# Kernel optimization log

Measured on AMD Instinct MI355X. Metric: run time of the kernel, lower is better.

The kernel has to match this reference:

```python
import jax, jax.numpy as jnp
import numpy as np

DIM = 512; HEADS = 8; HD = DIM // HEADS
B = 4; H = 32; W = 32; TXT = 77; LAT = 512
NE = 8; HID = 4 * DIM

def _ln(x, g, b):
    mu = jnp.mean(x, -1, keepdims=True)
    v = jnp.mean((x - mu) ** 2, -1, keepdims=True)
    return (x - mu) * jax.lax.rsqrt(v + 1e-5) * g + b

def _mha(q, k, v, in_w, in_b, out_w, out_b):
    # torch nn.MultiheadAttention (batch_first): packed in_proj, scaled dot-product, out_proj
    wq, wk, wv = jnp.split(in_w, 3, axis=0)
    bq, bk, bv = jnp.split(in_b, 3)
    sp = lambda t: t.reshape(t.shape[0], t.shape[1], HEADS, HD)
    Q = sp(q @ wq.T + bq) * (HD ** -0.5)
    K = sp(k @ wk.T + bk)
    V = sp(v @ wv.T + bv)
    att = jax.nn.softmax(jnp.einsum('bqhd,bkhd->bhqk', Q, K), axis=-1)
    o = jnp.einsum('bhqk,bkhd->bqhd', att, V).reshape(q.shape[0], q.shape[1], DIM)
    return o @ out_w.T + out_b

def _modconv1x1(x, weight, mod_w, mod_b, w_lat):
    # ModulatedConv with kernel_size=1: per-sample modulated + demodulated 1x1 conv == batched matmul
    style = w_lat @ mod_w.T + mod_b              # [B, Cin]
    wt = weight[None] * style[:, None, :]        # [B, Cout, Cin]
    wt = wt * jax.lax.rsqrt(jnp.sum(wt ** 2, axis=2, keepdims=True) + 1e-8)
    return jnp.einsum('boi,bihw->bohw', wt, x)

def _forward(x, w, text_seq, pin_weight, pin_mod_w, pin_mod_b, pout_weight, pout_mod_w, pout_mod_b,
             ln1_g, ln1_b, ln2_g, ln2_b, ln3_g, ln3_b,
             sa_in_w, sa_in_b, sa_out_w, sa_out_b, ca_in_w, ca_in_b, ca_out_w, ca_out_b,
             r_feat_mu, r_text_mu, r_comb_mu, r_temp, e_w1, e_b1, e_w2, e_b2):
    x_in = _modconv1x1(x, pin_weight, pin_mod_w, pin_mod_b, w)
    x_flat = x_in.transpose(0, 2, 3, 1).reshape(B, H * W, DIM)
    xn = _ln(x_flat, ln1_g, ln1_b)
    x_flat = x_flat + _mha(xn, xn, xn, sa_in_w, sa_in_b, sa_out_w, sa_out_b)
    xn = _ln(x_flat, ln2_g, ln2_b)
    x_flat = x_flat + _mha(xn, text_seq, text_seq, ca_in_w, ca_in_b, ca_out_w, ca_out_b)
    # SparseMoE (eval mode): Bayesian router uses mean weights, hard top-1 one-hot routing
    tok = _ln(x_flat, ln3_g, ln3_b).reshape(B * H * W, DIM)
    w_tok = jnp.repeat(w, H * W, axis=0)                      # [N, LAT]
    combined = jnp.concatenate([tok @ r_feat_mu, w_tok @ r_text_mu], axis=1)  # [N, 256]
    logits = (combined @ r_comb_mu) / jnp.clip(r_temp, 0.1, None)
    probs = jax.nn.softmax(logits, axis=1)
    one_hot = jax.nn.one_hot(jnp.argmax(probs, axis=1), NE, dtype=probs.dtype)  # [N, NE]
    hdn = jax.nn.gelu(jnp.einsum('nd,edh->neh', tok, e_w1) + e_b1, approximate=False)
    expert_out = jnp.einsum('neh,ehd->ned', hdn, e_w2) + e_b2  # [N, NE, DIM]
    moe = jnp.einsum('ne,ned->nd', one_hot, expert_out)
    x_flat = x_flat + moe.reshape(B, H * W, DIM)
    x_sp = x_flat.reshape(B, H, W, DIM).transpose(0, 3, 1, 2)
    x_out = _modconv1x1(x_sp, pout_weight, pout_mod_w, pout_mod_b, w)
    return x_out, one_hot

def setup_inputs():
    key = jax.random.key(0)
    ks = jax.random.split(key, 20)
    r = lambda i, shape, s=1.0: jax.random.normal(ks[i], shape, jnp.float32) * s
    z = lambda *shape: jnp.zeros(shape, jnp.float32)
    o = lambda *shape: jnp.ones(shape, jnp.float32)
    return {
        'x': r(0, (B, DIM, H, W)),
        'w': r(1, (B, LAT)),
        'text_seq': r(2, (B, TXT, DIM)),
        'pin_weight': r(3, (DIM, DIM), 0.05), 'pin_mod_w': r(4, (DIM, LAT), 0.02), 'pin_mod_b': z(DIM),
        'pout_weight': r(5, (DIM, DIM), 0.05), 'pout_mod_w': r(6, (DIM, LAT), 0.02), 'pout_mod_b': z(DIM),
        'ln1_g': o(DIM), 'ln1_b': z(DIM), 'ln2_g': o(DIM), 'ln2_b': z(DIM), 'ln3_g': o(DIM), 'ln3_b': z(DIM),
        'sa_in_w': r(7, (3 * DIM, DIM), 0.03), 'sa_in_b': z(3 * DIM),
        'sa_out_w': r(8, (DIM, DIM), 0.03), 'sa_out_b': z(DIM),
        'ca_in_w': r(9, (3 * DIM, DIM), 0.03), 'ca_in_b': z(3 * DIM),
        'ca_out_w': r(10, (DIM, DIM), 0.03), 'ca_out_b': z(DIM),
        'r_feat_mu': r(11, (DIM, 128), 0.1), 'r_text_mu': r(12, (LAT, 128), 0.1),
        'r_comb_mu': r(13, (256, NE), 0.1), 'r_temp': o(1),
        'e_w1': r(14, (NE, DIM, HID), 0.02), 'e_b1': z(NE, HID),
        'e_w2': r(15, (NE, HID, DIM), 0.02), 'e_b2': z(NE, DIM),
    }

def reference(x, w, text_seq, pin_weight, pin_mod_w, pin_mod_b, pout_weight, pout_mod_w, pout_mod_b,
              ln1_g, ln1_b, ln2_g, ln2_b, ln3_g, ln3_b,
              sa_in_w, sa_in_b, sa_out_w, sa_out_b, ca_in_w, ca_in_b, ca_out_w, ca_out_b,
              r_feat_mu, r_text_mu, r_comb_mu, r_temp, e_w1, e_b1, e_w2, e_b2):
    return _forward(x, w, text_seq, pin_weight, pin_mod_w, pin_mod_b, pout_weight, pout_mod_w, pout_mod_b,
                    ln1_g, ln1_b, ln2_g, ln2_b, ln3_g, ln3_b,
                    sa_in_w, sa_in_b, sa_out_w, sa_out_b, ca_in_w, ca_in_b, ca_out_w, ca_out_b,
                    r_feat_mu, r_text_mu, r_comb_mu, r_temp, e_w1, e_b1, e_w2, e_b2)
```

## Files before the change

kernel.cpp:

```cpp
#include <hip/hip_runtime.h>
#include <hip/hip_bf16.h>
#include <math.h>

#define DIMC 512
#define HEADS 8
#define HD 64
#define BB 4
#define HWX 1024
#define TXT 77
#define LATC 512
#define NE 8
#define HIDC 2048
#define NTOK 4096
#define MAXT 72

typedef __attribute__((ext_vector_type(8))) short bf16x8;
typedef __attribute__((ext_vector_type(4))) float f32x4;
typedef __hip_bfloat16 bf16;

__device__ __forceinline__ void split2(float v, bf16& h, bf16& l) {
    h = __float2bfloat16(v);
    l = __float2bfloat16(v - __bfloat162float(h));
}
__device__ __forceinline__ void split2s(float v, short& h, short& l) {
// ... 180 lines not shown
        *(bf16x8*)&BsL[bufo + t * 8] = vbl;
        __syncthreads();
        int kn = (kk + 32 < K) ? kk + 32 : kk;
        bf16x8 nah = *(const bf16x8*)(AbH + aoff + kn);
        bf16x8 nal = *(const bf16x8*)(AbL + aoff + kn);
        bf16x8 nbh = *(const bf16x8*)(BbH + boff + kn);
        bf16x8 nbl = *(const bf16x8*)(BbL + boff + kn);
        bf16x8 aH[2], aL[2], bH[2], bL[2];
        #pragma unroll
        for (int i = 0; i < 2; i++) {
            aH[i] = *(const bf16x8*)&AsH[bufo + aOff[i]];
            aL[i] = *(const bf16x8*)&AsL[bufo + aOff[i]];
            bH[i] = *(const bf16x8*)&BsH[bufo + bOff[i]];
            bL[i] = *(const bf16x8*)&BsL[bufo + bOff[i]];
        }
        #pragma unroll
        for (int i = 0; i < 2; i++)
        #pragma unroll
        for (int j = 0; j < 2; j++) {
            acc[i][j] = __builtin_amdgcn_mfma_f32_16x16x32_bf16(aH[i], bH[j], acc[i][j], 0, 0, 0);
            acc[i][j] = __builtin_amdgcn_mfma_f32_16x16x32_bf16(aH[i], bL[j], acc[i][j], 0, 0, 0);
            acc[i][j] = __builtin_amdgcn_mfma_f32_16x16x32_bf16(aL[i], bH[j], acc[i][j], 0, 0, 0);
        }
        vah = nah; val = nal; vbh = nbh; vbl = nbl;
        bufo ^= 2048;
    }
    #pragma unroll
    for (int i = 0; i < 2; i++)
    #pragma unroll
    for (int j = 0; j < 2; j++)
    #pragma unroll
    for (int r = 0; r < 4; r++) {
        int row = bm + wm + i * 16 + fq * 4 + r;
        int col = bn + wn + j * 16 + fr;
        if (row < M) {
            long off = (long)row * cs_m + (long)col * cs_n;
            float v = acc[i][j][r];
            if (bias) v += bias[col];
            if (Oh) {
                bf16 hh, ll; split2(v, hh, ll);
                Oh[off] = hh; Ol[off] = ll;
            } else {
                if (Rb) v += Rb[off];
                Cb[off] = v;
            }
        }
    }
}

__global__ __launch_bounds__(256) void mgemm128x64_kernel(
    const bf16* __restrict__ Ah, const bf16* __restrict__ Al,
    const bf16* __restrict__ Bh, const bf16* __restrict__ Bl,
    const float* __restrict__ bias, bf16* __restrict__ Oh, bf16* __restrict__ Ol,
    int M, int N, int K) {
    __shared__ short AsH[2 * 4096];
    __shared__ short AsL[2 * 4096];
    __shared__ short BsH[2 * 2048];
    __shared__ short BsL[2 * 2048];
    const short* AbH = (const short*)Ah;
    const short* AbL = (const short*)Al;
    const short* BbH = (const short*)Bh;
    const short* BbL = (const short*)Bl;
    int bm = blockIdx.y * 128, bn = blockIdx.x * 64;
    int t = threadIdx.x, lane = t & 63, w = t >> 6;
    int wm = (w >> 1) * 64, wn = (w & 1) * 32;
    int p0 = t, p1 = t + 256;
    int ra0 = p0 >> 2, ka0 = (p0 & 3) ^ ((ra0 >> 1) & 3);
    int ra1 = p1 >> 2, ka1 = (p1 & 3) ^ ((ra1 >> 1) & 3);
    int arow0 = bm + ra0; if (arow0 > M - 1) arow0 = M - 1;
    int arow1 = bm + ra1; if (arow1 > M - 1) arow1 = M - 1;
    long aoff0 = (long)arow0 * K + ka0 * 8;
    long aoff1 = (long)arow1 * K + ka1 * 8;
    int rb = t >> 2, kb2 = (t & 3) ^ ((rb >> 1) & 3);
    long boff = (long)(bn + rb) * K + kb2 * 8;
    int fr = lane & 15, fq = lane >> 4;
    int aOff[4], bOff[2];
    #pragma unroll
    for (int i = 0; i < 4; i++) {
        int row = wm + i * 16 + fr;
        aOff[i] = row * 32 + ((fq ^ ((row >> 1) & 3)) * 8);
    }
    #pragma unroll
    for (int j = 0; j < 2; j++) {
        int col = wn + j * 16 + fr;
        bOff[j] = col * 32 + ((fq ^ ((col >> 1) & 3)) * 8);
    }
    f32x4 acc[4][2] = {};
    bf16x8 vah0 = *(const bf16x8*)(AbH + aoff0);
    bf16x8 vah1 = *(const bf16x8*)(AbH + aoff1);
    bf16x8 val0 = *(const bf16x8*)(AbL + aoff0);
    bf16x8 val1 = *(const bf16x8*)(AbL + aoff1);
    bf16x8 vbh  = *(const bf16x8*)(BbH + boff);
    bf16x8 vbl  = *(const bf16x8*)(BbL + boff);
    int bufA = 0, bufB = 0;
    for (int kk = 0; kk < K; kk += 32) {
        *(bf16x8*)&AsH[bufA + p0 * 8] = vah0;  *(bf16x8*)&AsH[bufA + p1 * 8] = vah1;
        *(bf16x8*)&AsL[bufA + p0 * 8] = val0;  *(bf16x8*)&AsL[bufA + p1 * 8] = val1;
        *(bf16x8*)&BsH[bufB + t * 8] = vbh;
        *(bf16x8*)&BsL[bufB + t * 8] = vbl;
        __syncthreads();
        int kn = (kk + 32 < K) ? kk + 32 : kk;
        bf16x8 nah0 = *(const bf16x8*)(AbH + aoff0 + kn);
        bf16x8 nah1 = *(const bf16x8*)(AbH + aoff1 + kn);
        bf16x8 nal0 = *(const bf16x8*)(AbL + aoff0 + kn);
        bf16x8 nal1 = *(const bf16x8*)(AbL + aoff1 + kn);
        bf16x8 nbh  = *(const bf16x8*)(BbH + boff + kn);
        bf16x8 nbl  = *(const bf16x8*)(BbL + boff + kn);
        bf16x8 aH[4], aL[4], bH[2], bL[2];
        #pragma unroll
        for (int i = 0; i < 4; i++) {
            aH[i] = *(const bf16x8*)&AsH[bufA + aOff[i]];
            aL[i] = *(const bf16x8*)&AsL[bufA + aOff[i]];
        }
        #pragma unroll
        for (int j = 0; j < 2; j++) {
            bH[j] = *(const bf16x8*)&BsH[bufB + bOff[j]];
            bL[j] = *(const bf16x8*)&BsL[bufB + bOff[j]];
        }
        #pragma unroll
        for (int i = 0; i < 4; i++)
        #pragma unroll
        for (int j = 0; j < 2; j++) {
            acc[i][j] = __builtin_amdgcn_mfma_f32_16x16x32_bf16(aH[i], bH[j], acc[i][j], 0, 0, 0);
            acc[i][j] = __builtin_amdgcn_mfma_f32_16x16x32_bf16(aH[i], bL[j], acc[i][j], 0, 0, 0);
            acc[i][j] = __builtin_amdgcn_mfma_f32_16x16x32_bf16(aL[i], bH[j], acc[i][j], 0, 0, 0);
        }
        vah0 = nah0; vah1 = nah1; val0 = nal0; val1 = nal1;
        vbh = nbh; vbl = nbl;
        bufA ^= 4096; bufB ^= 2048;
    }
    #pragma unroll
    for (int i = 0; i < 4; i++)
    #pragma unroll
    for (int j = 0; j < 2; j++)
    #pragma unroll
    for (int r = 0; r < 4; r++) {
        int row = bm + wm + i * 16 + fq * 4 + r;
        int col = bn + wn + j * 16 + fr;
        if (row < M) {
            long off = (long)row * N + col;
            float v = acc[i][j][r] + bias[col];
            bf16 hh, ll; split2(v, hh, ll);
            Oh[off] = hh; Ol[off] = ll;
        }
    }
}

__global__ __launch_bounds__(256) void sa_mfma_kernel(
    const bf16* __restrict__ qh, const bf16* __restrict__ ql,
    bf16* __restrict__ oh, bf16* __restrict__ ol) {
    int qt = blockIdx.x, h = blockIdx.y, b = blockIdx.z;
    __shared__ short KsH[4096], KsL[4096];
    __shared__ short VtH[4608], VtL[4608];
    __shared__ short PHs[4][1024], PLs[4][1024];
    int t = threadIdx.x, lane = t & 63, w = t >> 6;
    int fr = lane & 15, fq = lane >> 4;
    const short* QH = (const short*)qh;
    const short* QL = (const short*)ql;
    long qrow = (long)(b * 1024 + qt * 64 + w * 16 + fr) * 1536 + h * 64;
    bf16x8 Qh2[2], Ql2[2];
    Qh2[0] = *(const bf16x8*)(QH + qrow + fq * 8);
    Qh2[1] = *(const bf16x8*)(QH + qrow + 32 + fq * 8);
    Ql2[0] = *(const bf16x8*)(QL + qrow + fq * 8);
    Ql2[1] = *(const bf16x8*)(QL + qrow + 32 + fq * 8);
    float l_i[4] = {0.f, 0.f, 0.f, 0.f};
    f32x4 o_acc[4] = {};
    int c0 = t, c1 = t + 256;
    int r0 = c0 >> 3, g0 = c0 & 7;
    int r1 = c1 >> 3, g1 = c1 & 7;
    int kd0 = r0 * 64 + ((g0 * 8) ^ ((r0 & 7) << 3));
    int kd1 = r1 * 64 + ((g1 * 8) ^ ((r1 & 7) << 3));
    long kb = (long)(b * 1024) * 1536 + 512 + h * 64;
    long vb = kb + 512;
    long lo0 = (long)r0 * 1536 + g0 * 8, lo1 = (long)r1 * 1536 + g1 * 8;
    short* ph = PHs[w]; short* pl = PLs[w];
    bf16x8 kh0 = *(const bf16x8*)(QH + kb + lo0);
    bf16x8 kh1 = *(const bf16x8*)(QH + kb + lo1);
    bf16x8 kl0 = *(const bf16x8*)(QL + kb + lo0);
    bf16x8 kl1 = *(const bf16x8*)(QL + kb + lo1);
    bf16x8 vh0 = *(const bf16x8*)(QH + vb + lo0);
    bf16x8 vh1 = *(const bf16x8*)(QH + vb + lo1);
    bf16x8 vl0 = *(const bf16x8*)(QL + vb + lo0);
    bf16x8 vl1 = *(const bf16x8*)(QL + vb + lo1);
    for (int kt = 0; kt < 16; kt++) {
        __syncthreads();
        *(bf16x8*)&KsH[kd0] = kh0;  *(bf16x8*)&KsH[kd1] = kh1;
        *(bf16x8*)&KsL[kd0] = kl0;  *(bf16x8*)&KsL[kd1] = kl1;
        #pragma unroll
        for (int j = 0; j < 8; j++) {
            int d0 = g0 * 8 + j;
            int i0 = d0 * 72 + (r0 ^ (g0 << 3));
            VtH[i0] = ((short*)&vh0)[j];  VtL[i0] = ((short*)&vl0)[j];
            int d1 = g1 * 8 + j;
            int i1 = d1 * 72 + (r1 ^ (g1 << 3));
            VtH[i1] = ((short*)&vh1)[j];  VtL[i1] = ((short*)&vl1)[j];
        }
        __syncthreads();
        int ktn = (kt + 1 < 16) ? kt + 1 : kt;
        long ko = kb + (long)(ktn * 64) * 1536;
        long vo = vb + (long)(ktn * 64) * 1536;
        bf16x8 nkh0 = *(const bf16x8*)(QH + ko + lo0);
        bf16x8 nkh1 = *(const bf16x8*)(QH + ko + lo1);
        bf16x8 nkl0 = *(const bf16x8*)(QL + ko + lo0);
        bf16x8 nkl1 = *(const bf16x8*)(QL + ko + lo1);
        bf16x8 nvh0 = *(const bf16x8*)(QH + vo + lo0);
        bf16x8 nvh1 = *(const bf16x8*)(QH + vo + lo1);
        bf16x8 nvl0 = *(const bf16x8*)(QL + vo + lo0);
        bf16x8 nvl1 = *(const bf16x8*)(QL + vo + lo1);
        __builtin_amdgcn_s_setprio(1);
        f32x4 s[4] = {};
        #pragma unroll
        for (int cf = 0; cf < 4; cf++) {
            int kvrow = cf * 16 + fr;
            #pragma unroll
            for (int kf = 0; kf < 2; kf++) {
                int idx = kvrow * 64 + ((kf * 32 + fq * 8) ^ ((kvrow & 7) << 3));
                bf16x8 Bh2 = *(const bf16x8*)&KsH[idx];
                bf16x8 Bl2 = *(const bf16x8*)&KsL[idx];
                s[cf] = __builtin_amdgcn_mfma_f32_16x16x32_bf16(Qh2[kf], Bh2, s[cf], 0, 0, 0);
                s[cf] = __builtin_amdgcn_mfma_f32_16x16x32_bf16(Qh2[kf], Bl2, s[cf], 0, 0, 0);
                s[cf] = __builtin_amdgcn_mfma_f32_16x16x32_bf16(Ql2[kf], Bh2, s[cf], 0, 0, 0);
            }
        }
        __builtin_amdgcn_s_setprio(0);
        #pragma unroll
        for (int cf = 0; cf < 4; cf++)
        #pragma unroll
        for (int reg = 0; reg < 4; reg++) {
            float e = __expf(s[cf][reg] * 0.125f);
            s[cf][reg] = e;
            l_i[reg] += e;
        }
        #pragma unroll
        for (int cf = 0; cf < 4; cf++)
        #pragma unroll
        for (int reg = 0; reg < 4; reg++) {
            int q = fq * 4 + reg, kv = cf * 16 + fr;
            int idx = q * 64 + (kv ^ ((q & 7) << 3));
            split2s(s[cf][reg], ph[idx], pl[idx]);
        }
        asm volatile("s_waitcnt lgkmcnt(0)" ::: "memory");
        __builtin_amdgcn_sched_barrier(0);
        __builtin_amdgcn_s_setprio(1);
        bf16x8 Pf_h[2], Pf_l[2];
        #pragma unroll
        for (int kf = 0; kf < 2; kf++) {
            int idx = fr * 64 + ((kf * 32 + fq * 8) ^ ((fr & 7) << 3));
            Pf_h[kf] = *(const bf16x8*)&ph[idx];
            Pf_l[kf] = *(const bf16x8*)&pl[idx];
        }
        #pragma unroll
        for (int cf = 0; cf < 4; cf++) {
            int d = cf * 16 + fr;
            #pragma unroll
            for (int kf = 0; kf < 2; kf++) {
                int idx = d * 72 + ((kf * 32 + fq * 8) ^ (((d >> 3) & 7) << 3));
                bf16x8 Vh2 = *(const bf16x8*)&VtH[idx];
                bf16x8 Vl2 = *(const bf16x8*)&VtL[idx];
                o_acc[cf] = __builtin_amdgcn_mfma_f32_16x16x32_bf16(Pf_h[kf], Vh2, o_acc[cf], 0, 0, 0);
                o_acc[cf] = __builtin_amdgcn_mfma_f32_16x16x32_bf16(Pf_h[kf], Vl2, o_acc[cf], 0, 0, 0);
                o_acc[cf] = __builtin_amdgcn_mfma_f32_16x16x32_bf16(Pf_l[kf], Vh2, o_acc[cf], 0, 0, 0);
            }
        }
        __builtin_amdgcn_s_setprio(0);
        kh0 = nkh0; kh1 = nkh1; kl0 = nkl0; kl1 = nkl1;
        vh0 = nvh0; vh1 = nvh1; vl0 = nvl0; vl1 = nvl1;
    }
    #pragma unroll
    for (int reg = 0; reg < 4; reg++) {
        float rs = l_i[reg];
        rs += __shfl_xor(rs, 1);
        rs += __shfl_xor(rs, 2);
        rs += __shfl_xor(rs, 4);
        rs += __shfl_xor(rs, 8);
        float inv = 1.f / rs;
        long m = (long)(b * 1024 + qt * 64 + w * 16 + fq * 4 + reg);
        #pragma unroll
        for (int cf = 0; cf < 4; cf++) {
            float v = o_acc[cf][reg] * inv;
            bf16 hh, ll; split2(v, hh, ll);
            long off = m * DIMC + h * 64 + cf * 16 + fr;
            oh[off] = hh; ol[off] = ll;
        }
    }
}

__global__ __launch_bounds__(256) void ca_mfma_kernel(
    const bf16* __restrict__ qh, const bf16* __restrict__ ql,
    const bf16* __restrict__ kvh, const bf16* __restrict__ kvl,
    bf16* __restrict__ oh, bf16* __restrict__ ol) {
    int qt = blockIdx.x, h = blockIdx.y, b = blockIdx.z;
    __shared__ short UH[8192], UL[8192];
    __shared__ short PHs[4][2048], PLs[4][2048];
    int t = threadIdx.x, lane = t & 63, w = t >> 6;
    int fr = lane & 15, fq = lane >> 4;
    const short* QH = (const short*)qh;
    const short* QL = (const short*)ql;
    const short* KVH = (const short*)kvh;
    const short* KVL = (const short*)kvl;
    long qrow = (long)(b * 1024 + qt * 64 + w * 16 + fr) * DIMC + h * 64;
    bf16x8 Qh2[2], Ql2[2];
    Qh2[0] = *(const bf16x8*)(QH + qrow + fq * 8);
    Qh2[1] = *(const bf16x8*)(QH + qrow + 32 + fq * 8);
    Ql2[0] = *(const bf16x8*)(QL + qrow + fq * 8);
    Ql2[1] = *(const bf16x8*)(QL + qrow + 32 + fq * 8);
    for (int c = t; c < 768; c += 256) {
        int r = c >> 3, g = c & 7;
        int idx = r * 64 + ((g * 8) ^ ((r & 7) << 3));
        bf16x8 vh = {}, vl = {};
        if (r < 77) {
            long src = (long)(b * 77 + r) * 1024 + h * 64 + g * 8;
            vh = *(const bf16x8*)(KVH + src);
            vl = *(const bf16x8*)(KVL + src);
        }
        *(bf16x8*)&UH[idx] = vh;
        *(bf16x8*)&UL[idx] = vl;
    }
    __syncthreads();
    f32x4 s[5] = {};
    #pragma unroll
    for (int cf = 0; cf < 5; cf++) {
        int kvrow = cf * 16 + fr;
        #pragma unroll
        for (int kf = 0; kf < 2; kf++) {
            int idx = kvrow * 64 + ((kf * 32 + fq * 8) ^ ((kvrow & 7) << 3));
            bf16x8 Bh2 = *(const bf16x8*)&UH[idx];
            bf16x8 Bl2 = *(const bf16x8*)&UL[idx];
            s[cf] = __builtin_amdgcn_mfma_f32_16x16x32_bf16(Qh2[kf], Bh2, s[cf], 0, 0, 0);
            s[cf] = __builtin_amdgcn_mfma_f32_16x16x32_bf16(Qh2[kf], Bl2, s[cf], 0, 0, 0);
            s[cf] = __builtin_amdgcn_mfma_f32_16x16x32_bf16(Ql2[kf], Bh2, s[cf], 0, 0, 0);
        }
    }
    float inv[4];
    #pragma unroll
    for (int reg = 0; reg < 4; reg++) {
        float rs = 0.f;
        #pragma unroll
        for (int cf = 0; cf < 5; cf++) {
            int kv = cf * 16 + fr;
            float e = (kv < 77) ? __expf(s[cf][reg] * 0.125f) : 0.f;
            s[cf][reg] = e;
            rs += e;
        }
        rs += __shfl_xor(rs, 1);
        rs += __shfl_xor(rs, 2);
        rs += __shfl_xor(rs, 4);
        rs += __shfl_xor(rs, 8);
        inv[reg] = 1.f / rs;
    }
    short* ph = PHs[w]; short* pl = PLs[w];
    #pragma unroll
    for (int cf = 0; cf < 6; cf++)
    #pragma unroll
    for (int reg = 0; reg < 4; reg++) {
        int q = fq * 4 + reg, kv = cf * 16 + fr;
        int idx = q * 128 + (kv ^ ((q & 7) << 3));
        float pv = (cf < 5) ? s[cf][reg] * inv[reg] : 0.f;
        split2s(pv, ph[idx], pl[idx]);
    }
    __syncthreads();
    for (int c = t; c < 768; c += 256) {
        int r = c >> 3, g = c & 7;
        bf16x8 vh = {}, vl = {};
        if (r < 77) {
            long src = (long)(b * 77 + r) * 1024 + 512 + h * 64 + g * 8;
            vh = *(const bf16x8*)(KVH + src);
            vl = *(const bf16x8*)(KVL + src);
        }
        #pragma unroll
        for (int j = 0; j < 8; j++) {
            int d = g * 8 + j;
            int idx = d * 128 + (r ^ (((d >> 3) & 7) << 3));
            UH[idx] = ((short*)&vh)[j];
            UL[idx] = ((short*)&vl)[j];
        }
    }
    __syncthreads();
    f32x4 o_acc[4] = {};
    bf16x8 Pf_h[3], Pf_l[3];
    #pragma unroll
    for (int kf = 0; kf < 3; kf++) {
        int idx = fr * 128 + ((kf * 32 + fq * 8) ^ ((fr & 7) << 3));
        Pf_h[kf] = *(const bf16x8*)&ph[idx];
        Pf_l[kf] = *(const bf16x8*)&pl[idx];
    }
    #pragma unroll
    for (int cf = 0; cf < 4; cf++) {
        int d = cf * 16 + fr;
        #pragma unroll
        for (int kf = 0; kf < 3; kf++) {
            int idx = d * 128 + ((kf * 32 + fq * 8) ^ (((d >> 3) & 7) << 3));
            bf16x8 Vh2 = *(const bf16x8*)&UH[idx];
            bf16x8 Vl2 = *(const bf16x8*)&UL[idx];
            o_acc[cf] = __builtin_amdgcn_mfma_f32_16x16x32_bf16(Pf_h[kf], Vh2, o_acc[cf], 0, 0, 0);
            o_acc[cf] = __builtin_amdgcn_mfma_f32_16x16x32_bf16(Pf_h[kf], Vl2, o_acc[cf], 0, 0, 0);
            o_acc[cf] = __builtin_amdgcn_mfma_f32_16x16x32_bf16(Pf_l[kf], Vh2, o_acc[cf], 0, 0, 0);
        }
    }
    #pragma unroll
    for (int reg = 0; reg < 4; reg++) {
        long m = (long)(b * 1024 + qt * 64 + w * 16 + fq * 4 + reg);
        #pragma unroll
        for (int cf = 0; cf < 4; cf++) {
            bf16 hh, ll; split2(o_acc[cf][reg], hh, ll);
            long off = m * DIMC + h * 64 + cf * 16 + fr;
            oh[off] = hh; ol[off] = ll;
        }
    }
}

__global__ __launch_bounds__(256) void moe64_1_kernel(
    const bf16* __restrict__ xn_b, const bf16* __restrict__ e1T, const float* __restrict__ e_b1,
    const int* __restrict__ table, const int* __restrict__ ntiles, const int* __restrict__ perm,
    bf16* __restrict__ hid_b) {
    if (blockIdx.y >= ntiles[0]) return;
    int e = table[2 * blockIdx.y], row0 = table[2 * blockIdx.y + 1];
    int bn = blockIdx.x * 64;
    __shared__ short As[2 * 2048];
    __shared__ short Bs[2 * 2048];
    __shared__ int rowsS[64];
    int t = threadIdx.x, lane = t & 63, w = t >> 6;
    if (t < 64) rowsS[t] = perm[row0 + t];
    __syncthreads();
    int wm = (w >> 1) * 32, wn = (w & 1) * 32;
    int r0 = t >> 2, k0s = (t & 3) ^ ((r0 >> 1) & 3);
    int tok0 = rowsS[r0]; if (tok0 < 0) tok0 = 0;
    const short* Xs = (const short*)xn_b;
    const short* Ws = (const short*)(e1T + (long)e * HIDC * DIMC);
    const short* a0 = Xs + (long)tok0 * DIMC + k0s * 8;
    const short* b0 = Ws + (long)(bn + r0) * DIMC + k0s * 8;
    int fr = lane & 15, fq = lane >> 4;
    int aOff[2], bOff[2];
    #pragma unroll
    for (int i = 0; i < 2; i++) {
        int row = wm + i * 16 + fr;
        aOff[i] = row * 32 + ((fq ^ ((row >> 1) & 3)) * 8);
        int col = wn + i * 16 + fr;
        bOff[i] = col * 32 + ((fq ^ ((col >> 1) & 3)) * 8);
    }
    f32x4 acc[2][2] = {};
    bf16x8 va = *(const bf16x8*)(a0);
    bf16x8 vb = *(const bf16x8*)(b0);
    int bufo = 0;
    for (int kk = 0; kk < DIMC; kk += 32) {
        *(bf16x8*)&As[bufo + t * 8] = va;
        *(bf16x8*)&Bs[bufo + t * 8] = vb;
        __syncthreads();
        int kn = (kk + 32 < DIMC) ? kk + 32 : kk;
        bf16x8 na = *(const bf16x8*)(a0 + kn);
        bf16x8 nb = *(const bf16x8*)(b0 + kn);
        bf16x8 aF[2], bF[2];
        #pragma unroll
        for (int i = 0; i < 2; i++) {
            aF[i] = *(const bf16x8*)&As[bufo + aOff[i]];
            bF[i] = *(const bf16x8*)&Bs[bufo + bOff[i]];
        }
        #pragma unroll
        for (int i = 0; i < 2; i++)
        #pragma unroll
        for (int j = 0; j < 2; j++)
            acc[i][j] = __builtin_amdgcn_mfma_f32_16x16x32_bf16(aF[i], bF[j], acc[i][j], 0, 0, 0);
        va = na; vb = nb;
        bufo ^= 2048;
    }
    const float* bb = e_b1 + (long)e * HIDC;
    #pragma unroll
    for (int i = 0; i < 2; i++)
    #pragma unroll
    for (int r = 0; r < 4; r++) {
        int tok = rowsS[wm + i * 16 + fq * 4 + r];
        if (tok < 0) continue;
        #pragma unroll
        for (int j = 0; j < 2; j++) {
            int col = bn + wn + j * 16 + fr;
            float v = acc[i][j][r] + bb[col];
            v = 0.5f * v * (1.f + erff(v * 0.70710678f));
            hid_b[(long)tok * HIDC + col] = __float2bfloat16(v);
        }
    }
}

__global__ __launch_bounds__(256) void moe64_2_kernel(
    const bf16* __restrict__ hid_b, const bf16* __restrict__ e2T, const float* __restrict__ e_b2,
    const int* __restrict__ table, const int* __restrict__ ntiles, const int* __restrict__ perm,
    const float* __restrict__ resid, bf16* __restrict__ outh, bf16* __restrict__ outl) {
    if (blockIdx.y >= ntiles[0]) return;
    int e = table[2 * blockIdx.y], row0 = table[2 * blockIdx.y + 1];
    int bn = blockIdx.x * 64;
    __shared__ short As[2 * 2048];
    __shared__ short Bs[2 * 2048];
    __shared__ int rowsS[64];
    int t = threadIdx.x, lane = t & 63, w = t >> 6;
    if (t < 64) rowsS[t] = perm[row0 + t];
    __syncthreads();
    int wm = (w >> 1) * 32, wn = (w & 1) * 32;
    int r0 = t >> 2, k0s = (t & 3) ^ ((r0 >> 1) & 3);
    int tok0 = rowsS[r0]; if (tok0 < 0) tok0 = 0;
    const short* Hs = (const short*)hid_b;
    const short* Ws = (const short*)(e2T + (long)e * DIMC * HIDC);
    const short* a0 = Hs + (long)tok0 * HIDC + k0s * 8;
    const short* b0 = Ws + (long)(bn + r0) * HIDC + k0s * 8;
    int fr = lane & 15, fq = lane >> 4;
    int aOff[2], bOff[2];
    #pragma unroll
    for (int i = 0; i < 2; i++) {
        int row = wm + i * 16 + fr;
        aOff[i] = row * 32 + ((fq ^ ((row >> 1) & 3)) * 8);
        int col = wn + i * 16 + fr;
        bOff[i] = col * 32 + ((fq ^ ((col >> 1) & 3)) * 8);
    }
    f32x4 acc[2][2] = {};
    bf16x8 va = *(const bf16x8*)(a0);
    bf16x8 vb = *(const bf16x8*)(b0);
    int bufo = 0;
    for (int kk = 0; kk < HIDC; kk += 32) {
        *(bf16x8*)&As[bufo + t * 8] = va;
        *(bf16x8*)&Bs[bufo + t * 8] = vb;
        __syncthreads();
        int kn = (kk + 32 < HIDC) ? kk + 32 : kk;
        bf16x8 na = *(const bf16x8*)(a0 + kn);
        bf16x8 nb = *(const bf16x8*)(b0 + kn);
        bf16x8 aF[2], bF[2];
        #pragma unroll
        for (int i = 0; i < 2; i++) {
            aF[i] = *(const bf16x8*)&As[bufo + aOff[i]];
            bF[i] = *(const bf16x8*)&Bs[bufo + bOff[i]];
        }
        #pragma unroll
        for (int i = 0; i < 2; i++)
        #pragma unroll
        for (int j = 0; j < 2; j++)
            acc[i][j] = __builtin_amdgcn_mfma_f32_16x16x32_bf16(aF[i], bF[j], acc[i][j], 0, 0, 0);
        va = na; vb = nb;
        bufo ^= 2048;
    }
    const float* bb = e_b2 + (long)e * DIMC;
    #pragma unroll
    for (int i = 0; i < 2; i++)
    #pragma unroll
    for (int r = 0; r < 4; r++) {
        int tok = rowsS[wm + i * 16 + fq * 4 + r];
        if (tok < 0) continue;
        #pragma unroll
        for (int j = 0; j < 2; j++) {
            int col = bn + wn + j * 16 + fr;
            long off = (long)tok * DIMC + col;
            float v = resid[off] + acc[i][j][r] + bb[col];
            bf16 hh, ll; split2(v, hh, ll);
            outh[off] = hh; outl[off] = ll;
        }
    }
}

__global__ void ln_kernel(const float* __restrict__ x, const float* __restrict__ g,
                          const float* __restrict__ b, float* __restrict__ y,
                          bf16* __restrict__ yh, bf16* __restrict__ yl) {
    int tok = blockIdx.x;
    int t = threadIdx.x;
    const float* xr = x + (long)tok * DIMC;
    float v0 = xr[t], v1 = xr[t + 256];
    __shared__ float red[256];
    red[t] = v0 + v1; __syncthreads();
    for (int s = 128; s > 0; s >>= 1) { if (t < s) red[t] += red[t + s]; __syncthreads(); }
    float mu = red[0] * (1.f / DIMC);
    __syncthreads();
    float d0 = v0 - mu, d1 = v1 - mu;
    red[t] = d0 * d0 + d1 * d1; __syncthreads();
    for (int s = 128; s > 0; s >>= 1) { if (t < s) red[t] += red[t + s]; __syncthreads(); }
    float rs = rsqrtf(red[0] * (1.f / DIMC) + 1e-5f);
    float o0 = d0 * rs * g[t] + b[t];
    float o1 = d1 * rs * g[t + 256] + b[t + 256];
    if (y) { y[(long)tok * DIMC + t] = o0; y[(long)tok * DIMC + t + 256] = o1; }
    bf16 h, l;
    split2(o0, h, l); yh[(long)tok * DIMC + t] = h;       yl[(long)tok * DIMC + t] = l;
    split2(o1, h, l); yh[(long)tok * DIMC + t + 256] = h; yl[(long)tok * DIMC + t + 256] = l;
}

__global__ void textpart_kernel(const float* __restrict__ w, const float* __restrict__ r_text_mu,
                                const float* __restrict__ r_comb_mu, float* __restrict__ tp,
                                int* __restrict__ cnt) {
    __shared__ float tw[4][128];
    int t = threadIdx.x;
    if (t < NE) cnt[t] = 0;
    for (int j = 0; j < 2; j++) {
        int idx = t + j * 256; int b = idx >> 7, c = idx & 127;
        const float* wr = w + (long)b * LATC;
        float s = 0.f;
        for (int k = 0; k < LATC; k++) s += wr[k] * r_text_mu[(long)k * 128 + c];
        tw[b][c] = s;
    }
    __syncthreads();
    if (t < 32) {
        int b = t >> 3, e = t & 7;
        float s = 0.f;
        for (int c = 0; c < 128; c++) s += tw[b][c] * r_comb_mu[(long)(128 + c) * 8 + e];
        tp[t] = s;
    }
}

__global__ void route_kernel(const float* __restrict__ feat, const float* __restrict__ tp,
                             const float* __restrict__ r_comb_mu, const float* __restrict__ r_temp,
                             float* __restrict__ onehot, int* __restrict__ idx, int* __restrict__ cnt,
                             int* __restrict__ perm) {
    int n = blockIdx.x * blockDim.x + threadIdx.x;
    if (n < MAXT * 64) perm[n] = -1;
    if (n >= NTOK) return;
    int b = n >> 10;
    float tmp = fmaxf(r_temp[0], 0.1f);
    float invt = 1.f / tmp;
    const float* fr = feat + (long)n * 128;
    float lg[8];
    for (int e = 0; e < 8; e++) {
        float s = 0.f;
        for (int c = 0; c < 128; c++) s += fr[c] * r_comb_mu[(long)c * 8 + e];
        lg[e] = (s + tp[b * 8 + e]) * invt;
    }
    float best = lg[0]; int bi = 0;
    for (int e = 1; e < 8; e++) { if (lg[e] > best) { best = lg[e]; bi = e; } }
    for (int e = 0; e < 8; e++) onehot[(long)n * 8 + e] = (e == bi) ? 1.f : 0.f;
    idx[n] = bi;
    atomicAdd(&cnt[bi], 1);
}

__global__ void offscatter_kernel(const int* __restrict__ cnt, const int* __restrict__ idx,
                                  int* __restrict__ ntiles, int* __restrict__ table,
                                  int* __restrict__ perm) {
    __shared__ int cur[NE];
    int t = threadIdx.x;
    if (t == 0) {
        int po = 0, nt = 0;
        for (int e = 0; e < NE; e++) {
            cur[e] = po;
            int tiles = (cnt[e] + 63) >> 6;
            for (int j = 0; j < tiles; j++) { table[2 * nt] = e; table[2 * nt + 1] = po + j * 64; nt++; }
            po += tiles * 64;
        }
        ntiles[0] = nt;
    }
    __syncthreads();
    for (int n = t; n < NTOK; n += 256) {
        int e = idx[n];
        int pos = atomicAdd(&cur[e], 1);
        perm[pos] = n;
    }
}

extern "C" void kernel_launch(void* const* d_in, const int* in_sizes, int n_in,
                              void* d_out, int out_size, void* d_ws, size_t ws_size,
                              hipStream_t stream) {
    const float* x        = (const float*)d_in[0];
    const float* w        = (const float*)d_in[1];
    const float* text     = (const float*)d_in[2];
    const float* pin_w    = (const float*)d_in[3];
    const float* pin_mw   = (const float*)d_in[4];
    const float* pin_mb   = (const float*)d_in[5];
    const float* pout_w   = (const float*)d_in[6];
    const float* pout_mw  = (const float*)d_in[7];
    const float* pout_mb  = (const float*)d_in[8];
    const float* ln1g     = (const float*)d_in[9];
    const float* ln1b     = (const float*)d_in[10];
    const float* ln2g     = (const float*)d_in[11];
    const float* ln2b     = (const float*)d_in[12];
    const float* ln3g     = (const float*)d_in[13];
    const float* ln3b     = (const float*)d_in[14];
    const float* sa_in_w  = (const float*)d_in[15];
    const float* sa_in_b  = (const float*)d_in[16];
    const float* sa_out_w = (const float*)d_in[17];
    const float* sa_out_b = (const float*)d_in[18];
    const float* ca_in_w  = (const float*)d_in[19];
    const float* ca_in_b  = (const float*)d_in[20];
    const float* ca_out_w = (const float*)d_in[21];
    const float* ca_out_b = (const float*)d_in[22];
    const float* r_feat   = (const float*)d_in[23];
    const float* r_text   = (const float*)d_in[24];
    const float* r_comb   = (const float*)d_in[25];
    const float* r_temp   = (const float*)d_in[26];
    const float* e_w1     = (const float*)d_in[27];
    const float* e_b1     = (const float*)d_in[28];
    const float* e_w2     = (const float*)d_in[29];
    const float* e_b2     = (const float*)d_in[30];

    float* out    = (float*)d_out;
    float* onehot = out + (long)BB * DIMC * HWX;

    float* f32p = (float*)d_ws;
    float* style_in  = f32p;
    float* style_out = f32p + 2048;
    float* tp        = f32p + 4096;
    int*   idx       = (int*)(f32p + 4128);
    int*   cnt       = (int*)(f32p + 8224);
    int*   ntiles    = (int*)(f32p + 8240);
    int*   table     = (int*)(f32p + 8248);
    int*   perm      = (int*)(f32p + 8504);
    float* x_flat    = f32p + 13496;
    float* xn        = x_flat + 2097152;
    float* qkv       = xn + 2097152;
    float* spill     = qkv + 6291456;

    bf16* bp = (bf16*)(f32p + 12596408);
    bf16* R1 = bp;
    bf16* xT_h  = R1;
    bf16* xT_l  = R1 + 2097152;
    bf16* wtA_h = R1 + 4194304;
    bf16* wtA_l = R1 + 5242880;
    bf16* obuf_h = R1;
    bf16* obuf_l = R1 + 2097152;
    bf16* kvt_h  = R1 + 4194304;
    bf16* kvt_l  = kvt_h + 315392;
    float* feat  = (float*)(kvt_l + 315392);
    bf16* xn_h = R1 + 6291456;
    bf16* xn_l = xn_h + 2097152;
    bf16* WB   = xn_l + 2097152;
    bf16* text_h   = WB;
    bf16* text_l   = text_h + 157696;
    bf16* sawin_h  = text_l + 157696;
    bf16* sawin_l  = sawin_h + 786432;
    bf16* sawout_h = sawin_l + 786432;
    bf16* sawout_l = sawout_h + 262144;
    bf16* caw_h    = sawout_l + 262144;
    bf16* caw_l    = caw_h + 786432;
    bf16* cawout_h = caw_l + 786432;
    bf16* cawout_l = cawout_h + 262144;
    bf16* rfT_h    = cawout_l + 262144;
    bf16* rfT_l    = rfT_h + 65536;
    bf16* hid_b    = WB;
    bf16* e1T = (bf16*)qkv;
    bf16* e2T = e1T + 8388608;
    bf16* xfl_h = xn_h;
    bf16* xfl_l = xn_l;
    bf16* wtC_h = (bf16*)xn;
    bf16* wtC_l = wtC_h + 1048576;
    bf16* q_h = (bf16*)qkv;
    bf16* q_l = q_h + 6291456;
    bf16* ca_qh = (bf16*)qkv;
    bf16* ca_ql = ca_qh + 2097152;
    (void)ws_size; (void)spill;

    auto mg = [&](const bf16* Ah, const bf16* Al, const bf16* Bh, const bf16* Bl,
                  const float* bias, const float* resid, float* C, bf16* Oh, bf16* Ol,
                  int M, int N, int K, long ab, long bb, long cb, int csm, int csn, int nb) {
        dim3 g(N / 64, (M + 63) / 64, nb);
        hipLaunchKernelGGL(mgemm64_kernel, g, dim3(256), 0, stream,
                           Ah, Al, Bh, Bl, bias, resid, C, Oh, Ol, M, N, K, ab, bb, cb, csm, csn);
    };

    {
        int n0 = 1536 * 512, n1 = 512 * 512, n2 = 1536 * 512, n3 = 512 * 512, n4 = BB * TXT * 512;
        int total = n0 + n1 + n2 + n3 + n4;
        hipLaunchKernelGGL(cvtall_kernel, dim3((total / 4 + 255) / 256), dim3(256), 0, stream,
                           sa_in_w, sawin_h, sawin_l, n0,
                           sa_out_w, sawout_h, sawout_l, n1,
                           ca_in_w, caw_h, caw_l, n2,
                           ca_out_w, cawout_h, cawout_l, n3,
                           text, text_h, text_l, n4);
    }
    hipLaunchKernelGGL(trcvt2x_kernel, dim3(32, 16, 5), dim3(256), 0, stream,
                       x, xT_h, xT_l, r_feat, rfT_h, rfT_l);

    hipLaunchKernelGGL(style2_kernel, dim3(16), dim3(256), 0, stream,
                       w, pin_mw, pin_mb, pout_mw, pout_mb, style_in, style_out);
    hipLaunchKernelGGL(wtmod2_kernel, dim3(2 * BB * DIMC), dim3(256), 0, stream,
                       pin_w, style_in, pout_w, style_out, wtA_h, wtA_l, wtC_h, wtC_l);

    mg(xT_h, xT_l, wtA_h, wtA_l, nullptr, nullptr, x_flat, nullptr, nullptr,
       HWX, DIMC, DIMC, (long)HWX * DIMC, (long)DIMC * DIMC, (long)HWX * DIMC, DIMC, 1, BB);

    hipLaunchKernelGGL(ln_kernel, dim3(NTOK), dim3(256), 0, stream, x_flat, ln1g, ln1b,
                       (float*)nullptr, xn_h, xn_l);
    hipLaunchKernelGGL(mgemm128x64_kernel, dim3(1536 / 64, NTOK / 128), dim3(256), 0, stream,
                       xn_h, xn_l, sawin_h, sawin_l, sa_in_b, q_h, q_l, NTOK, 1536, 512);
    hipLaunchKernelGGL(sa_mfma_kernel, dim3(16, HEADS, BB), dim3(256), 0, stream,
                       q_h, q_l, obuf_h, obuf_l);
    mg(obuf_h, obuf_l, sawout_h, sawout_l, sa_out_b, x_flat, x_flat, nullptr, nullptr,
       NTOK, 512, 512, 0, 0, 0, 512, 1, 1);

    hipLaunchKernelGGL(ln_kernel, dim3(NTOK), dim3(256), 0, stream, x_flat, ln2g, ln2b,
                       (float*)nullptr, xn_h, xn_l);
    mg(xn_h, xn_l, caw_h, caw_l, ca_in_b, nullptr, nullptr, ca_qh, ca_ql,
       NTOK, 512, 512, 0, 0, 0, 512, 1, 1);
    mg(text_h, text_l, caw_h + 512 * 512, caw_l + 512 * 512, ca_in_b + 512, nullptr, nullptr,
       kvt_h, kvt_l, BB * TXT, 1024, 512, 0, 0, 0, 1024, 1, 1);
    hipLaunchKernelGGL(ca_mfma_kernel, dim3(16, HEADS, BB), dim3(256), 0, stream,
                       ca_qh, ca_ql, kvt_h, kvt_l, obuf_h, obuf_l);
    hipLaunchKernelGGL(tr2x_kernel, dim3(64, 16, 16), dim3(256), 0, stream,
                       e_w1, e1T, e_w2, e2T);
    mg(obuf_h, obuf_l, cawout_h, cawout_l, ca_out_b, x_flat, x_flat, nullptr, nullptr,
       NTOK, 512, 512, 0, 0, 0, 512, 1, 1);

    hipLaunchKernelGGL(ln_kernel, dim3(NTOK), dim3(256), 0, stream, x_flat, ln3g, ln3b,
                       (float*)nullptr, xn_h, xn_l);
    mg(xn_h, xn_l, rfT_h, rfT_l, nullptr, nullptr, feat, nullptr, nullptr,
       NTOK, 128, 512, 0, 0, 0, 128, 1, 1);
    hipLaunchKernelGGL(textpart_kernel, dim3(1), dim3(256), 0, stream, w, r_text, r_comb, tp, cnt);
    hipLaunchKernelGGL(route_kernel, dim3(18), dim3(256), 0, stream,
                       feat, tp, r_comb, r_temp, onehot, idx, cnt, perm);
    hipLaunchKernelGGL(offscatter_kernel, dim3(1), dim3(256), 0, stream,
                       cnt, idx, ntiles, table, perm);

    hipLaunchKernelGGL(moe64_1_kernel, dim3(HIDC / 64, MAXT), dim3(256), 0, stream,
                       xn_h, e1T, e_b1, table, ntiles, perm, hid_b);
    hipLaunchKernelGGL(moe64_2_kernel, dim3(DIMC / 64, MAXT), dim3(256), 0, stream,
                       hid_b, e2T, e_b2, table, ntiles, perm, x_flat, xfl_h, xfl_l);

    mg(wtC_h, wtC_l, xfl_h, xfl_l, nullptr, nullptr, out, nullptr, nullptr,
       DIMC, HWX, DIMC, (long)DIMC * DIMC, (long)HWX * DIMC, (long)DIMC * HWX, HWX, 1, BB);
}
```

Before: 496.5 us.

## Drop low-half split of attention probabilities and widen MoE GEMM tiles to 128

The self- and cross-attention kernels now store softmax probabilities only as single bf16 instead of a hi/lo split. This removes one of three MFMAs in each PV product and halves the P shared-memory traffic. In self-attention the row sum is accumulated from the rounded values so normalization stays consistent. The two MoE expert GEMM kernels widen their N tile from 64 to 128 per block, giving each wave a 32x64 output and more MFMA work per A-tile load, with fewer blocks launched. The cost is lower precision in the attention output and possibly lower occupancy in the MoE kernels from the extra accumulators and shared memory.

```diff
diff --git a/kernel.cpp b/kernel.cpp
--- a/kernel.cpp
+++ b/kernel.cpp
@@ -356,7 +356,7 @@
     int qt = blockIdx.x, h = blockIdx.y, b = blockIdx.z;
     __shared__ short KsH[4096], KsL[4096];
     __shared__ short VtH[4608], VtL[4608];
-    __shared__ short PHs[4][1024], PLs[4][1024];
+    __shared__ short PHs[4][1024];
     int t = threadIdx.x, lane = t & 63, w = t >> 6;
     int fr = lane & 15, fq = lane >> 4;
     const short* QH = (const short*)qh;
@@ -377,7 +377,7 @@
     long kb = (long)(b * 1024) * 1536 + 512 + h * 64;
     long vb = kb + 512;
     long lo0 = (long)r0 * 1536 + g0 * 8, lo1 = (long)r1 * 1536 + g1 * 8;
-    short* ph = PHs[w]; short* pl = PLs[w];
+    short* ph = PHs[w];
     bf16x8 kh0 = *(const bf16x8*)(QH + kb + lo0);
     bf16x8 kh1 = *(const bf16x8*)(QH + kb + lo1);
     bf16x8 kl0 = *(const bf16x8*)(QL + kb + lo0);
@@ -432,26 +432,20 @@
         #pragma unroll
         for (int reg = 0; reg < 4; reg++) {
             float e = __expf(s[cf][reg] * 0.125f);
-            s[cf][reg] = e;
-            l_i[reg] += e;
-        }
-        #pragma unroll
-        for (int cf = 0; cf < 4; cf++)
-        #pragma unroll
-        for (int reg = 0; reg < 4; reg++) {
+            bf16 eb = __float2bfloat16(e);
+            l_i[reg] += __bfloat162float(eb);
             int q = fq * 4 + reg, kv = cf * 16 + fr;
             int idx = q * 64 + (kv ^ ((q & 7) << 3));
-            split2s(s[cf][reg], ph[idx], pl[idx]);
+            ph[idx] = *(short*)&eb;
         }
         asm volatile("s_waitcnt lgkmcnt(0)" ::: "memory");
         __builtin_amdgcn_sched_barrier(0);
         __builtin_amdgcn_s_setprio(1);
-        bf16x8 Pf_h[2], Pf_l[2];
+        bf16x8 Pf_h[2];
         #pragma unroll
         for (int kf = 0; kf < 2; kf++) {
             int idx = fr * 64 + ((kf * 32 + fq * 8) ^ ((fr & 7) << 3));
             Pf_h[kf] = *(const bf16x8*)&ph[idx];
-            Pf_l[kf] = *(const bf16x8*)&pl[idx];
         }
         #pragma unroll
         for (int cf = 0; cf < 4; cf++) {
@@ -463,7 +457,6 @@
                 bf16x8 Vl2 = *(const bf16x8*)&VtL[idx];
                 o_acc[cf] = __builtin_amdgcn_mfma_f32_16x16x32_bf16(Pf_h[kf], Vh2, o_acc[cf], 0, 0, 0);
                 o_acc[cf] = __builtin_amdgcn_mfma_f32_16x16x32_bf16(Pf_h[kf], Vl2, o_acc[cf], 0, 0, 0);
-                o_acc[cf] = __builtin_amdgcn_mfma_f32_16x16x32_bf16(Pf_l[kf], Vh2, o_acc[cf], 0, 0, 0);
             }
         }
         __builtin_amdgcn_s_setprio(0);
@@ -495,7 +488,7 @@
     bf16* __restrict__ oh, bf16* __restrict__ ol) {
     int qt = blockIdx.x, h = blockIdx.y, b = blockIdx.z;
     __shared__ short UH[8192], UL[8192];
-    __shared__ short PHs[4][2048], PLs[4][2048];
+    __shared__ short PHs[4][2048];
     int t = threadIdx.x, lane = t & 63, w = t >> 6;
     int fr = lane & 15, fq = lane >> 4;
     const short* QH = (const short*)qh;
@@ -552,7 +545,7 @@
         rs += __shfl_xor(rs, 8);
         inv[reg] = 1.f / rs;
     }
-    short* ph = PHs[w]; short* pl = PLs[w];
+    short* ph = PHs[w];
     #pragma unroll
     for (int cf = 0; cf < 6; cf++)
     #pragma unroll
@@ -560,7 +553,8 @@
         int q = fq * 4 + reg, kv = cf * 16 + fr;
         int idx = q * 128 + (kv ^ ((q & 7) << 3));
         float pv = (cf < 5) ? s[cf][reg] * inv[reg] : 0.f;
-        split2s(pv, ph[idx], pl[idx]);
+        bf16 pb = __float2bfloat16(pv);
+        ph[idx] = *(short*)&pb;
     }
     __syncthreads();
     for (int c = t; c < 768; c += 256) {
@@ -581,12 +575,11 @@
     }
     __syncthreads();
     f32x4 o_acc[4] = {};
-    bf16x8 Pf_h[3], Pf_l[3];
+    bf16x8 Pf_h[3];
     #pragma unroll
     for (int kf = 0; kf < 3; kf++) {
         int idx = fr * 128 + ((kf * 32 + fq * 8) ^ ((fr & 7) << 3));
         Pf_h[kf] = *(const bf16x8*)&ph[idx];
-        Pf_l[kf] = *(const bf16x8*)&pl[idx];
     }
     #pragma unroll
     for (int cf = 0; cf < 4; cf++) {
@@ -598,7 +591,6 @@
             bf16x8 Vl2 = *(const bf16x8*)&UL[idx];
             o_acc[cf] = __builtin_amdgcn_mfma_f32_16x16x32_bf16(Pf_h[kf], Vh2, o_acc[cf], 0, 0, 0);
             o_acc[cf] = __builtin_amdgcn_mfma_f32_16x16x32_bf16(Pf_h[kf], Vl2, o_acc[cf], 0, 0, 0);
-            o_acc[cf] = __builtin_amdgcn_mfma_f32_16x16x32_bf16(Pf_l[kf], Vh2, o_acc[cf], 0, 0, 0);
         }
     }
     #pragma unroll
@@ -613,59 +605,68 @@
     }
 }
 
-__global__ __launch_bounds__(256) void moe64_1_kernel(
+__global__ __launch_bounds__(256) void moe128_1_kernel(
     const bf16* __restrict__ xn_b, const bf16* __restrict__ e1T, const float* __restrict__ e_b1,
     const int* __restrict__ table, const int* __restrict__ ntiles, const int* __restrict__ perm,
     bf16* __restrict__ hid_b) {
     if (blockIdx.y >= ntiles[0]) return;
     int e = table[2 * blockIdx.y], row0 = table[2 * blockIdx.y + 1];
-    int bn = blockIdx.x * 64;
+    int bn = blockIdx.x * 128;
     __shared__ short As[2 * 2048];
-    __shared__ short Bs[2 * 2048];
+    __shared__ short Bs[2 * 4096];
     __shared__ int rowsS[64];
     int t = threadIdx.x, lane = t & 63, w = t >> 6;
     if (t < 64) rowsS[t] = perm[row0 + t];
     __syncthreads();
-    int wm = (w >> 1) * 32, wn = (w & 1) * 32;
-    int r0 = t >> 2, k0s = (t & 3) ^ ((r0 >> 1) & 3);
-    int tok0 = rowsS[r0]; if (tok0 < 0) tok0 = 0;
+    int wm = (w >> 1) * 32, wn = (w & 1) * 64;
+    int ra = t >> 2, ka = (t & 3) ^ ((ra >> 1) & 3);
+    int tok0 = rowsS[ra]; if (tok0 < 0) tok0 = 0;
     const short* Xs = (const short*)xn_b;
     const short* Ws = (const short*)(e1T + (long)e * HIDC * DIMC);
-    const short* a0 = Xs + (long)tok0 * DIMC + k0s * 8;
-    const short* b0 = Ws + (long)(bn + r0) * DIMC + k0s * 8;
+    const short* a0 = Xs + (long)tok0 * DIMC + ka * 8;
+    int p0 = t, p1 = t + 256;
+    int rb0 = p0 >> 2, kb0 = (p0 & 3) ^ ((rb0 >> 1) & 3);
+    int rb1 = p1 >> 2, kb1 = (p1 & 3) ^ ((rb1 >> 1) & 3);
+    const short* b0 = Ws + (long)(bn + rb0) * DIMC + kb0 * 8;
+    const short* b1 = Ws + (long)(bn + rb1) * DIMC + kb1 * 8;
     int fr = lane & 15, fq = lane >> 4;
-    int aOff[2], bOff[2];
+    int aOff[2], bOff[4];
     #pragma unroll
     for (int i = 0; i < 2; i++) {
         int row = wm + i * 16 + fr;
         aOff[i] = row * 32 + ((fq ^ ((row >> 1) & 3)) * 8);
-        int col = wn + i * 16 + fr;
-        bOff[i] = col * 32 + ((fq ^ ((col >> 1) & 3)) * 8);
-    }
-    f32x4 acc[2][2] = {};
-    bf16x8 va = *(const bf16x8*)(a0);
-    bf16x8 vb = *(const bf16x8*)(b0);
-    int bufo = 0;
+    }
+    #pragma unroll
+    for (int j = 0; j < 4; j++) {
+        int col = wn + j * 16 + fr;
+        bOff[j] = col * 32 + ((fq ^ ((col >> 1) & 3)) * 8);
+    }
+    f32x4 acc[2][4] = {};
+    bf16x8 va  = *(const bf16x8*)a0;
+    bf16x8 vb0 = *(const bf16x8*)b0;
+    bf16x8 vb1 = *(const bf16x8*)b1;
+    int bufA = 0, bufB = 0;
     for (int kk = 0; kk < DIMC; kk += 32) {
-        *(bf16x8*)&As[bufo + t * 8] = va;
-        *(bf16x8*)&Bs[bufo + t * 8] = vb;
+        *(bf16x8*)&As[bufA + t * 8] = va;
+        *(bf16x8*)&Bs[bufB + p0 * 8] = vb0;
+        *(bf16x8*)&Bs[bufB + p1 * 8] = vb1;
         __syncthreads();
         int kn = (kk + 32 < DIMC) ? kk + 32 : kk;
-        bf16x8 na = *(const bf16x8*)(a0 + kn);
-        bf16x8 nb = *(const bf16x8*)(b0 + kn);
-        bf16x8 aF[2], bF[2];
-        #pragma unroll
-        for (int i = 0; i < 2; i++) {
-            aF[i] = *(const bf16x8*)&As[bufo + aOff[i]];
-            bF[i] = *(const bf16x8*)&Bs[bufo + bOff[i]];
-        }
+        bf16x8 na  = *(const bf16x8*)(a0 + kn);
+        bf16x8 nb0 = *(const bf16x8*)(b0 + kn);
+        bf16x8 nb1 = *(const bf16x8*)(b1 + kn);
+        bf16x8 aF[2], bF[4];
+        #pragma unroll
+        for (int i = 0; i < 2; i++) aF[i] = *(const bf16x8*)&As[bufA + aOff[i]];
+        #pragma unroll
+        for (int j = 0; j < 4; j++) bF[j] = *(const bf16x8*)&Bs[bufB + bOff[j]];
         #pragma unroll
         for (int i = 0; i < 2; i++)
         #pragma unroll
-        for (int j = 0; j < 2; j++)
+        for (int j = 0; j < 4; j++)
             acc[i][j] = __builtin_amdgcn_mfma_f32_16x16x32_bf16(aF[i], bF[j], acc[i][j], 0, 0, 0);
-        va = na; vb = nb;
-        bufo ^= 2048;
+        va = na; vb0 = nb0; vb1 = nb1;
+        bufA ^= 2048; bufB ^= 4096;
     }
     const float* bb = e_b1 + (long)e * HIDC;
     #pragma unroll
@@ -675,7 +676,7 @@
         int tok = rowsS[wm + i * 16 + fq * 4 + r];
         if (tok < 0) continue;
         #pragma unroll
-        for (int j = 0; j < 2; j++) {
+        for (int j = 0; j < 4; j++) {
             int col = bn + wn + j * 16 + fr;
             float v = acc[i][j][r] + bb[col];
             v = 0.5f * v * (1.f + erff(v * 0.70710678f));
@@ -684,59 +685,68 @@
     }
 }
 
-__global__ __launch_bounds__(256) void moe64_2_kernel(
+__global__ __launch_bounds__(256) void moe128_2_kernel(
     const bf16* __restrict__ hid_b, const bf16* __restrict__ e2T, const float* __restrict__ e_b2,
     const int* __restrict__ table, const int* __restrict__ ntiles, const int* __restrict__ perm,
     const float* __restrict__ resid, bf16* __restrict__ outh, bf16* __restrict__ outl) {
     if (blockIdx.y >= ntiles[0]) return;
     int e = table[2 * blockIdx.y], row0 = table[2 * blockIdx.y + 1];
-    int bn = blockIdx.x * 64;
+    int bn = blockIdx.x * 128;
     __shared__ short As[2 * 2048];
-    __shared__ short Bs[2 * 2048];
+    __shared__ short Bs[2 * 4096];
     __shared__ int rowsS[64];
     int t = threadIdx.x, lane = t & 63, w = t >> 6;
     if (t < 64) rowsS[t] = perm[row0 + t];
     __syncthreads();
-    int wm = (w >> 1) * 32, wn = (w & 1) * 32;
-    int r0 = t >> 2, k0s = (t & 3) ^ ((r0 >> 1) & 3);
-    int tok0 = rowsS[r0]; if (tok0 < 0) tok0 = 0;
+    int wm = (w >> 1) * 32, wn = (w & 1) * 64;
+    int ra = t >> 2, ka = (t & 3) ^ ((ra >> 1) & 3);
+    int tok0 = rowsS[ra]; if (tok0 < 0) tok0 = 0;
     const short* Hs = (const short*)hid_b;
     const short* Ws = (const short*)(e2T + (long)e * DIMC * HIDC);
-    const short* a0 = Hs + (long)tok0 * HIDC + k0s * 8;
-    const short* b0 = Ws + (long)(bn + r0) * HIDC + k0s * 8;
+    const short* a0 = Hs + (long)tok0 * HIDC + ka * 8;
+    int p0 = t, p1 = t + 256;
+    int rb0 = p0 >> 2, kb0 = (p0 & 3) ^ ((rb0 >> 1) & 3);
+    int rb1 = p1 >> 2, kb1 = (p1 & 3) ^ ((rb1 >> 1) & 3);
+    const short* b0 = Ws + (long)(bn + rb0) * HIDC + kb0 * 8;
+    const short* b1 = Ws + (long)(bn + rb1) * HIDC + kb1 * 8;
     int fr = lane & 15, fq = lane >> 4;
-    int aOff[2], bOff[2];
+    int aOff[2], bOff[4];
     #pragma unroll
     for (int i = 0; i < 2; i++) {
         int row = wm + i * 16 + fr;
         aOff[i] = row * 32 + ((fq ^ ((row >> 1) & 3)) * 8);
-        int col = wn + i * 16 + fr;
-        bOff[i] = col * 32 + ((fq ^ ((col >> 1) & 3)) * 8);
-    }
-    f32x4 acc[2][2] = {};
-    bf16x8 va = *(const bf16x8*)(a0);
-    bf16x8 vb = *(const bf16x8*)(b0);
-    int bufo = 0;
+    }
+    #pragma unroll
+    for (int j = 0; j < 4; j++) {
+        int col = wn + j * 16 + fr;
+        bOff[j] = col * 32 + ((fq ^ ((col >> 1) & 3)) * 8);
+    }
+    f32x4 acc[2][4] = {};
+    bf16x8 va  = *(const bf16x8*)a0;
+    bf16x8 vb0 = *(const bf16x8*)b0;
+    bf16x8 vb1 = *(const bf16x8*)b1;
+    int bufA = 0, bufB = 0;
     for (int kk = 0; kk < HIDC; kk += 32) {
-        *(bf16x8*)&As[bufo + t * 8] = va;
-        *(bf16x8*)&Bs[bufo + t * 8] = vb;
+        *(bf16x8*)&As[bufA + t * 8] = va;
+        *(bf16x8*)&Bs[bufB + p0 * 8] = vb0;
+        *(bf16x8*)&Bs[bufB + p1 * 8] = vb1;
         __syncthreads();
         int kn = (kk + 32 < HIDC) ? kk + 32 : kk;
-        bf16x8 na = *(const bf16x8*)(a0 + kn);
-        bf16x8 nb = *(const bf16x8*)(b0 + kn);
-        bf16x8 aF[2], bF[2];
-        #pragma unroll
-        for (int i = 0; i < 2; i++) {
-            aF[i] = *(const bf16x8*)&As[bufo + aOff[i]];
-            bF[i] = *(const bf16x8*)&Bs[bufo + bOff[i]];
-        }
+        bf16x8 na  = *(const bf16x8*)(a0 + kn);
+        bf16x8 nb0 = *(const bf16x8*)(b0 + kn);
+        bf16x8 nb1 = *(const bf16x8*)(b1 + kn);
+        bf16x8 aF[2], bF[4];
+        #pragma unroll
+        for (int i = 0; i < 2; i++) aF[i] = *(const bf16x8*)&As[bufA + aOff[i]];
+        #pragma unroll
+        for (int j = 0; j < 4; j++) bF[j] = *(const bf16x8*)&Bs[bufB + bOff[j]];
         #pragma unroll
         for (int i = 0; i < 2; i++)
         #pragma unroll
-        for (int j = 0; j < 2; j++)
+        for (int j = 0; j < 4; j++)
             acc[i][j] = __builtin_amdgcn_mfma_f32_16x16x32_bf16(aF[i], bF[j], acc[i][j], 0, 0, 0);
-        va = na; vb = nb;
-        bufo ^= 2048;
+        va = na; vb0 = nb0; vb1 = nb1;
+        bufA ^= 2048; bufB ^= 4096;
     }
     const float* bb = e_b2 + (long)e * DIMC;
     #pragma unroll
@@ -746,7 +756,7 @@
         int tok = rowsS[wm + i * 16 + fq * 4 + r];
         if (tok < 0) continue;
         #pragma unroll
-        for (int j = 0; j < 2; j++) {
+        for (int j = 0; j < 4; j++) {
             int col = bn + wn + j * 16 + fr;
             long off = (long)tok * DIMC + col;
             float v = resid[off] + acc[i][j][r] + bb[col];
@@ -1001,9 +1011,9 @@
     hipLaunchKernelGGL(offscatter_kernel, dim3(1), dim3(256), 0, stream,
                        cnt, idx, ntiles, table, perm);
 
-    hipLaunchKernelGGL(moe64_1_kernel, dim3(HIDC / 64, MAXT), dim3(256), 0, stream,
+    hipLaunchKernelGGL(moe128_1_kernel, dim3(HIDC / 128, MAXT), dim3(256), 0, stream,
                        xn_h, e1T, e_b1, table, ntiles, perm, hid_b);
-    hipLaunchKernelGGL(moe64_2_kernel, dim3(DIMC / 64, MAXT), dim3(256), 0, stream,
+    hipLaunchKernelGGL(moe128_2_kernel, dim3(DIMC / 128, MAXT), dim3(256), 0, stream,
                        hid_b, e2T, e_b2, table, ntiles, perm, x_flat, xfl_h, xfl_l);
 
     mg(wtC_h, wtC_l, xfl_h, xfl_l, nullptr, nullptr, out, nullptr, nullptr,
```

After: 488.5 us. No clear change (-1.6%).
